# Kernel optimization log

Measured on AMD Instinct MI355X. Metric: run time of the kernel, lower is better.

## Reference

```python
import jax, jax.numpy as jnp
import numpy as np

B = 128      # trees per batch
D = 10       # tree depth (perfect binary tree)
L = 2 ** D   # leaves per tree
V = 50000    # vocab
E = 300      # embed size
C = 5        # num classes


def setup_inputs() -> dict:
    key = jax.random.key(0)
    k0, k1, k2, k3 = jax.random.split(key, 4)
    return {
        "word_ids": jax.random.randint(k0, (B, L), 0, V),
        "embedding": jax.random.normal(k1, (V, E), jnp.float32) * 0.02,
        "W_w": jax.random.normal(k2, (E, 2 * E), jnp.float32) * (1.0 / np.sqrt(2 * E)),
        "W_b": jnp.zeros((E,), jnp.float32),
        "P_w": jax.random.normal(k3, (C, E), jnp.float32) * (1.0 / np.sqrt(E)),
        "P_b": jnp.zeros((C,), jnp.float32),
    }


def reference(word_ids, embedding, W_w, W_b, P_w, P_b):
    # Leaf nodes: relu(Embedding(word))  -> [B, L, E]
    h = jax.nn.relu(embedding[word_ids])
    # projection of every node (torch Linear: x @ W.T + b)
    logits = [jnp.einsum("bne,ce->bnc", h, P_w) + P_b]
    # Combine same-depth sibling pairs level by level (D fixed levels).
    for _ in range(D):
        pair = jnp.concatenate([h[:, 0::2], h[:, 1::2]], axis=-1)  # [B, n/2, 2E]
        h = jax.nn.relu(jnp.einsum("bnf,ef->bne", pair, W_w) + W_b)  # [B, n/2, E]
        logits.append(jnp.einsum("bne,ce->bnc", h, P_w) + P_b)
    # All node logits, leaves first then each internal level up to the root.
    return jnp.concatenate(logits, axis=1)  # [B, 2L-1, C]
```

## Files before the change

kernel.cpp:

```cpp
#include <hip/hip_runtime.h>
#include <hip/hip_bf16.h>

#define B_ 128
#define D_ 10
#define L_ 1024
#define E_ 300
#define C_ 5
#define NODES 2047
#define HSTR 304
#define KP 608
#define NP 320
#define PK 320
#define LSTR 328

typedef __attribute__((ext_vector_type(8))) short short8;
typedef __attribute__((ext_vector_type(4))) float f32x4;
typedef __hip_bfloat16 bf16;

__device__ __forceinline__ short f2bs(float v) {
  bf16 b = (bf16)v;
  return *reinterpret_cast<short*>(&b);
}

__device__ __forceinline__ short8 pack_relu(f32x4 v0, f32x4 v1) {
  short8 s;
#pragma unroll
  for (int j = 0; j < 4; j++) s[j] = f2bs(fmaxf(v0[j], 0.f));
#pragma unroll
  for (int j = 0; j < 4; j++) s[4 + j] = f2bs(fmaxf(v1[j], 0.f));
  return s;
}

__global__ __launch_bounds__(256) void prep_k(
    const float* __restrict__ emb, const float* __restrict__ Ww,
    const float* __restrict__ Pw, bf16* __restrict__ T, bf16* __restrict__ Wp,
    bf16* __restrict__ Pp, bf16* __restrict__ Pq, int V) {
  int idx = blockIdx.x * 256 + threadIdx.x;
  int tchunks = V * 38;
  if (idx < tchunks) {
    int v = idx / 38, c = idx % 38;
    const float* src = emb + (size_t)v * E_ + c * 8;
    f32x4 v0 = *(const f32x4*)src;
    f32x4 v1;
    if (c == 37) v1 = (f32x4){0.f, 0.f, 0.f, 0.f};
    else v1 = *(const f32x4*)(src + 4);
    *(short8*)(T + (size_t)v * HSTR + c * 8) = pack_relu(v0, v1);
  }
  if (idx < NP * KP) {
    int r = idx / KP, c = idx % KP;
    float v = 0.f;
    if (r < E_) {
      if (c < E_) v = Ww[r * 600 + c];
      else if (c >= HSTR && c < HSTR + E_) v = Ww[r * 600 + (c - 4)];
    }
    Wp[idx] = (bf16)v;
  }
  if (idx < 16 * PK) {
    int r = idx / PK, c = idx % PK;
    float v = (r < C_ && c < E_) ? Pw[r * E_ + c] : 0.f;
    Pp[idx] = (bf16)v;
  }
  if (idx < 2 * 16 * KP) {
    int p = idx / (16 * KP);
    int rem = idx % (16 * KP);
    int r = rem / KP, c = rem % KP;
    int e = c - p * HSTR;
    float v = (r < C_ && e >= 0 && e < E_) ? Pw[r * E_ + e] : 0.f;
    Pq[idx] = (bf16)v;
  }
}

#define PROJ_A(rowptr, ks, k0)                                        \
  ((ks) == 9 && half >= 2 ? (short8){0, 0, 0, 0, 0, 0, 0, 0}          \
                          : *(const short8*)((rowptr) + (k0)))

__global__ __launch_bounds__(256, 4) void fused_l1_k(
    const int* __restrict__ wid, const bf16* __restrict__ T,
    const bf16* __restrict__ Wp, const float* __restrict__ Wb,
    const bf16* __restrict__ Pq, const bf16* __restrict__ Pp,
    const float* __restrict__ Pb, bf16* __restrict__ h1,
    float* __restrict__ out) {
  __shared__ bf16 hs[33][HSTR];
  int tid = threadIdx.x;
  int w = tid >> 6, l = tid & 63, q = l & 15, half = l >> 4;
  int m0 = blockIdx.x * 32;

  int mr0 = m0 + q, mr1 = m0 + 16 + q;
  int o0a = wid[2 * mr0] * HSTR, o0b = wid[2 * mr0 + 1] * HSTR;
  int o1a = wid[2 * mr1] * HSTR, o1b = wid[2 * mr1 + 1] * HSTR;

  int p = w & 1, rtl = w >> 1;

  f32x4 acc[2][5];
#pragma unroll
  for (int rt = 0; rt < 2; rt++)
#pragma unroll
    for (int nt = 0; nt < 5; nt++) acc[rt][nt] = (f32x4){0.f, 0.f, 0.f, 0.f};
  f32x4 pacc = (f32x4){0.f, 0.f, 0.f, 0.f};

#define LDA(ks, d0, d1)                                          \
  {                                                              \
    int k0_ = (ks) * 32 + half * 8;                              \
    int sel_ = k0_ >= HSTR;                                      \
    int e0_ = sel_ ? k0_ - HSTR : k0_;                           \
    d0 = *(const short8*)(T + (sel_ ? o0b : o0a) + e0_);         \
    d1 = *(const short8*)(T + (sel_ ? o1b : o1a) + e0_);         \
  }

  short8 aA0, aA1, aB0, aB1, aC0, aC1;
  LDA(0, aA0, aA1);
  LDA(1, aB0, aB1);

  for (int ks = 0; ks < 19; ks++) {
    int kn = ks + 2 <= 18 ? ks + 2 : 18;
    LDA(kn, aC0, aC1);
    int k0 = ks * 32 + half * 8;
    short8 al = rtl ? aA1 : aA0;
    short8 pqf = *(const short8*)(Pq + ((size_t)p * 16 + q) * KP + k0);
    pacc = __builtin_amdgcn_mfma_f32_16x16x32_bf16(al, pqf, pacc, 0, 0, 0);
#pragma unroll
    for (int nt = 0; nt < 5; nt++) {
      short8 b =
          *(const short8*)(Wp + (size_t)(w * 80 + nt * 16 + q) * KP + k0);
      acc[0][nt] =
          __builtin_amdgcn_mfma_f32_16x16x32_bf16(aA0, b, acc[0][nt], 0, 0, 0);
      acc[1][nt] =
          __builtin_amdgcn_mfma_f32_16x16x32_bf16(aA1, b, acc[1][nt], 0, 0, 0);
    }
    aA0 = aB0; aA1 = aB1;
    aB0 = aC0; aB1 = aC1;
  }
#undef LDA

#pragma unroll
  for (int nt = 0; nt < 5; nt++) {
    int n = w * 80 + nt * 16 + q;
    float wb = (n < E_) ? Wb[n] : 0.f;
    if (n < HSTR) {
#pragma unroll
      for (int rt = 0; rt < 2; rt++)
#pragma unroll
        for (int j = 0; j < 4; j++) {
          int rl = rt * 16 + half * 4 + j;
          hs[rl][n] = (bf16)fmaxf(acc[rt][nt][j] + wb, 0.f);
        }
    }
  }
  if (q < C_) {
    float pb = Pb[q];
#pragma unroll
    for (int j = 0; j < 4; j++) {
      int leaf = 2 * (m0 + rtl * 16 + half * 4 + j) + p;
      out[((size_t)(leaf >> 10) * NODES + (leaf & 1023)) * C_ + q] =
          pacc[j] + pb;
    }
  }
  __syncthreads();

  for (int i = tid; i < 32 * 38; i += 256) {
    int r = i / 38, c = i % 38;
    *(short8*)(h1 + (size_t)(m0 + r) * HSTR + c * 8) =
        *(const short8*)&hs[r][c * 8];
  }
  if (w < 2) {
    f32x4 pc = (f32x4){0.f, 0.f, 0.f, 0.f};
#pragma unroll
    for (int ks = 0; ks < 10; ks++) {
      int k0 = ks * 32 + half * 8;
      short8 a = PROJ_A(&hs[w * 16 + q][0], ks, k0);
      short8 b = *(const short8*)(Pp + (size_t)q * PK + k0);
      pc = __builtin_amdgcn_mfma_f32_16x16x32_bf16(a, b, pc, 0, 0, 0);
    }
    if (q < C_) {
      float pb = Pb[q];
#pragma unroll
      for (int j = 0; j < 4; j++) {
        int m = m0 + w * 16 + half * 4 + j;
        out[((size_t)(m >> 9) * NODES + 1024 + (m & 511)) * C_ + q] =
            pc[j] + pb;
      }
    }
  }
}

template <int RT>
__global__ __launch_bounds__(256, 4) void combine_k(
    const bf16* __restrict__ h_in, const bf16* __restrict__ Wp,
    const float* __restrict__ Wb, const bf16* __restrict__ Pp,
    const float* __restrict__ Pb, bf16* __restrict__ h_out,
    float* __restrict__ out, int node_off, int nshift) {
  __shared__ bf16 hs[RT * 16 + 1][HSTR];
  int tid = threadIdx.x;
  int w = tid >> 6, l = tid & 63, q = l & 15, half = l >> 4;
  size_t m0 = (size_t)blockIdx.x * (RT * 16);

  f32x4 acc[RT][5];
#pragma unroll
  for (int rt = 0; rt < RT; rt++)
#pragma unroll
    for (int nt = 0; nt < 5; nt++) acc[rt][nt] = (f32x4){0.f, 0.f, 0.f, 0.f};

  for (int ks = 0; ks < 19; ks++) {
    int k0 = ks * 32 + half * 8;
    short8 a[RT];
#pragma unroll
    for (int rt = 0; rt < RT; rt++)
      a[rt] = *(const short8*)(h_in + (m0 + rt * 16 + q) * KP + k0);
#pragma unroll
    for (int nt = 0; nt < 5; nt++) {
      short8 b =
          *(const short8*)(Wp + (size_t)(w * 80 + nt * 16 + q) * KP + k0);
#pragma unroll
      for (int rt = 0; rt < RT; rt++)
        acc[rt][nt] = __builtin_amdgcn_mfma_f32_16x16x32_bf16(a[rt], b,
                                                              acc[rt][nt], 0,
                                                              0, 0);
    }
  }

#pragma unroll
  for (int nt = 0; nt < 5; nt++) {
    int n = w * 80 + nt * 16 + q;
    float wb = (n < E_) ? Wb[n] : 0.f;
    if (n < HSTR) {
#pragma unroll
      for (int rt = 0; rt < RT; rt++)
#pragma unroll
        for (int j = 0; j < 4; j++) {
          int rl = rt * 16 + half * 4 + j;
          hs[rl][n] = (bf16)fmaxf(acc[rt][nt][j] + wb, 0.f);
        }
    }
  }
  __syncthreads();

  for (int i = tid; i < RT * 16 * 38; i += 256) {
    int r = i / 38, c = i % 38;
    *(short8*)(h_out + (m0 + r) * HSTR + c * 8) = *(const short8*)&hs[r][c * 8];
  }

  if (w < RT) {
    f32x4 pacc = (f32x4){0.f, 0.f, 0.f, 0.f};
#pragma unroll
    for (int ks = 0; ks < 10; ks++) {
      int k0 = ks * 32 + half * 8;
      short8 a = PROJ_A(&hs[16 * w + q][0], ks, k0);
      short8 b = *(const short8*)(Pp + (size_t)q * PK + k0);
      pacc = __builtin_amdgcn_mfma_f32_16x16x32_bf16(a, b, pacc, 0, 0, 0);
    }
    if (q < C_) {
      float pb = Pb[q];
#pragma unroll
      for (int j = 0; j < 4; j++) {
        size_t m = m0 + w * 16 + half * 4 + j;
        size_t b_ = m >> nshift;
        size_t n = m & (((size_t)1 << nshift) - 1);
        out[((size_t)b_ * NODES + node_off + n) * C_ + q] = pacc[j] + pb;
      }
    }
  }
}

__global__ __launch_bounds__(256) void tail_k(
    const bf16* __restrict__ h5, const bf16* __restrict__ Wp,
    const float* __restrict__ Wb, const bf16* __restrict__ Pp,
    const float* __restrict__ Pb, float* __restrict__ out) {
  __shared__ bf16 bufs[2][32][LSTR];
  int tid = threadIdx.x, b = blockIdx.x;
  int w = tid >> 6, l = tid & 63, q = l & 15, half = l >> 4;

  for (int i = tid; i < 32 * 38; i += 256) {
    int r = i / 38, c = i % 38;
    *(short8*)&bufs[0][r][c * 8] =
        *(const short8*)(h5 + ((size_t)b * 32 + r) * HSTR + c * 8);
  }
  __syncthreads();

  int p = 0, off = 2016, Mo = 16;
  for (int lev = 0; lev < 5; lev++) {
    f32x4 acc[5];
#pragma unroll
    for (int t = 0; t < 5; t++) acc[t] = (f32x4){0.f, 0.f, 0.f, 0.f};
    for (int ks = 0; ks < 19; ks++) {
      int k0 = ks * 32 + half * 8;
      int sel = k0 >= HSTR;
      int e0 = k0 - (sel ? HSTR : 0);
      short8 a = *(const short8*)&bufs[p][2 * q + sel][e0];
#pragma unroll
      for (int t = 0; t < 5; t++) {
        int nt = w + 4 * t;
        short8 bfr = *(const short8*)(Wp + ((size_t)nt * 16 + q) * KP + k0);
        acc[t] =
            __builtin_amdgcn_mfma_f32_16x16x32_bf16(a, bfr, acc[t], 0, 0, 0);
      }
    }
    __syncthreads();
#pragma unroll
    for (int t = 0; t < 5; t++) {
      int nt = w + 4 * t;
      int n = nt * 16 + q;
      float wb = (n < E_) ? Wb[n] : 0.f;
#pragma unroll
      for (int j = 0; j < 4; j++) {
        int r = half * 4 + j;
        bufs[p ^ 1][r][n] = (bf16)fmaxf(acc[t][j] + wb, 0.f);
      }
    }
    __syncthreads();
    if (w == 0) {
      f32x4 pc = (f32x4){0.f, 0.f, 0.f, 0.f};
#pragma unroll
      for (int ks = 0; ks < 10; ks++) {
        int k0 = ks * 32 + half * 8;
        short8 a = *(const short8*)&bufs[p ^ 1][q][k0];
        short8 bfr = *(const short8*)(Pp + (size_t)q * PK + k0);
        pc = __builtin_amdgcn_mfma_f32_16x16x32_bf16(a, bfr, pc, 0, 0, 0);
      }
      if (q < C_) {
        float pb = Pb[q];
#pragma unroll
        for (int j = 0; j < 4; j++) {
          int r = half * 4 + j;
          if (r < Mo) out[((size_t)b * NODES + off + r) * C_ + q] = pc[j] + pb;
        }
      }
    }
    p ^= 1;
    off += Mo;
    Mo >>= 1;
  }
}

extern "C" void kernel_launch(void* const* d_in, const int* in_sizes, int n_in,
                              void* d_out, int out_size, void* d_ws,
                              size_t ws_size, hipStream_t stream) {
  const int* wid = (const int*)d_in[0];
  const float* emb = (const float*)d_in[1];
  const float* Ww = (const float*)d_in[2];
  const float* Wb = (const float*)d_in[3];
  const float* Pw = (const float*)d_in[4];
  const float* Pb = (const float*)d_in[5];
  float* out = (float*)d_out;
  int V = in_sizes[1] / E_;

  bf16* hA = (bf16*)d_ws;
  bf16* hB = hA + (size_t)B_ * 512 * HSTR;
  bf16* Wp = hB + (size_t)B_ * 256 * HSTR;
  bf16* Pp = Wp + (size_t)NP * KP;
  bf16* Pq = Pp + (size_t)16 * PK;
  bf16* T = Pq + (size_t)2 * 16 * KP;

  int tchunks = V * 38;
  prep_k<<<(tchunks + 255) / 256, 256, 0, stream>>>(emb, Ww, Pw, T, Wp, Pp, Pq,
                                                    V);
  fused_l1_k<<<(B_ * 512) / 32, 256, 0, stream>>>(wid, T, Wp, Wb, Pq, Pp, Pb,
                                                  hA, out);
  combine_k<2><<<1024, 256, 0, stream>>>(hA, Wp, Wb, Pp, Pb, hB, out, 1536, 8);
  combine_k<2><<<512, 256, 0, stream>>>(hB, Wp, Wb, Pp, Pb, hA, out, 1792, 7);
  combine_k<1><<<512, 256, 0, stream>>>(hA, Wp, Wb, Pp, Pb, hB, out, 1920, 6);
  combine_k<1><<<256, 256, 0, stream>>>(hB, Wp, Wb, Pp, Pb, hA, out, 1984, 5);
  tail_k<<<B_, 256, 0, stream>>>(hA, Wp, Wb, Pp, Pb, out);
}
```

Baseline: 238.9 us.

## Drop full-vocab embedding prep, gather leaves in-kernel, use MFMA-fragment layouts

The prep kernel no longer converts the whole 50000x300 embedding table to bf16. It now only packs W and P into MFMA-fragment-ordered buffers. The level-1 kernel gathers and ReLU-converts the needed embedding rows directly into LDS and processes 64 rows per block. Intermediate activations are written in fragment order so later levels read contiguous 16-byte chunks per lane, and combine tile sizes are doubled. This removes a large pass over the embedding table, at the cost of more LDS and register pressure and lower occupancy.

```diff
diff --git a/kernel.cpp b/kernel.cpp
--- a/kernel.cpp
+++ b/kernel.cpp
@@ -2,16 +2,9 @@
 #include <hip/hip_bf16.h>
 
 #define B_ 128
-#define D_ 10
-#define L_ 1024
 #define E_ 300
 #define C_ 5
 #define NODES 2047
-#define HSTR 304
-#define KP 608
-#define NP 320
-#define PK 320
-#define LSTR 328
 
 typedef __attribute__((ext_vector_type(8))) short short8;
 typedef __attribute__((ext_vector_type(4))) float f32x4;
@@ -31,118 +24,143 @@
   return s;
 }
 
-__global__ __launch_bounds__(256) void prep_k(
-    const float* __restrict__ emb, const float* __restrict__ Ww,
-    const float* __restrict__ Pw, bf16* __restrict__ T, bf16* __restrict__ Wp,
-    bf16* __restrict__ Pp, bf16* __restrict__ Pq, int V) {
+#define HSROW(base, r) ((base) + (r) * 312)
+
+#define PROJ_A(rowptr, ks, k0)                               \
+  ((ks) == 9 && half >= 2 ? (short8){0, 0, 0, 0, 0, 0, 0, 0} \
+                          : *(const short8*)((rowptr) + (k0)))
+
+__global__ __launch_bounds__(256) void prep_k(const float* __restrict__ Ww,
+                                              const float* __restrict__ Pw,
+                                              bf16* __restrict__ Wf,
+                                              bf16* __restrict__ Pqf,
+                                              bf16* __restrict__ Ppf) {
   int idx = blockIdx.x * 256 + threadIdx.x;
-  int tchunks = V * 38;
-  if (idx < tchunks) {
-    int v = idx / 38, c = idx % 38;
-    const float* src = emb + (size_t)v * E_ + c * 8;
+  if (idx < 20 * 19 * 64) {
+    int wnt = idx / 1216, rem = idx % 1216;
+    int ks = rem >> 6, l = rem & 63;
+    int n = wnt * 16 + (l & 15);
+    int k0 = ks * 32 + (l >> 4) * 8;
+    short8 v;
+#pragma unroll
+    for (int j = 0; j < 8; j++) {
+      int k = k0 + j;
+      float x = 0.f;
+      if (n < E_) {
+        if (k < E_) x = Ww[n * 600 + k];
+        else if (k >= 304 && k < 604) x = Ww[n * 600 + k - 4];
+      }
+      v[j] = f2bs(x);
+    }
+    *(short8*)(Wf + (size_t)idx * 8) = v;
+  }
+  if (idx < 2 * 19 * 64) {
+    int p = idx / 1216, rem = idx % 1216;
+    int ks = rem >> 6, l = rem & 63;
+    int q = l & 15;
+    int k0 = ks * 32 + (l >> 4) * 8;
+    short8 v;
+#pragma unroll
+    for (int j = 0; j < 8; j++) {
+      int e = k0 + j - 304 * p;
+      float x = (q < C_ && e >= 0 && e < E_) ? Pw[q * E_ + e] : 0.f;
+      v[j] = f2bs(x);
+    }
+    *(short8*)(Pqf + (size_t)idx * 8) = v;
+  }
+  if (idx < 10 * 64) {
+    int ks = idx >> 6, l = idx & 63;
+    int q = l & 15;
+    int k0 = ks * 32 + (l >> 4) * 8;
+    short8 v;
+#pragma unroll
+    for (int j = 0; j < 8; j++) {
+      int e = k0 + j;
+      float x = (q < C_ && e < E_) ? Pw[q * E_ + e] : 0.f;
+      v[j] = f2bs(x);
+    }
+    *(short8*)(Ppf + (size_t)idx * 8) = v;
+  }
+}
+
+__global__ __launch_bounds__(256, 2) void fused_l1_k(
+    const int* __restrict__ wid, const float* __restrict__ emb,
+    const bf16* __restrict__ Wf, const float* __restrict__ Wb,
+    const bf16* __restrict__ Pqf, const bf16* __restrict__ Ppf,
+    const float* __restrict__ Pb, bf16* __restrict__ h1f,
+    float* __restrict__ out) {
+  __shared__ short ldsA[64 * 616 + 64];
+  int tid = threadIdx.x;
+  int m0 = blockIdx.x * 64;
+
+#pragma unroll 2
+  for (int it = 0; it < 19; ++it) {
+    int i = it * 256 + tid;
+    int r = i / 76, c2 = i % 76;
+    int par = c2 >= 38 ? 1 : 0;
+    int c = c2 - 38 * par;
+    int word = wid[2 * (m0 + r) + par];
+    const float* src = emb + (size_t)word * E_ + c * 8;
     f32x4 v0 = *(const f32x4*)src;
-    f32x4 v1;
-    if (c == 37) v1 = (f32x4){0.f, 0.f, 0.f, 0.f};
-    else v1 = *(const f32x4*)(src + 4);
-    *(short8*)(T + (size_t)v * HSTR + c * 8) = pack_relu(v0, v1);
-  }
-  if (idx < NP * KP) {
-    int r = idx / KP, c = idx % KP;
-    float v = 0.f;
-    if (r < E_) {
-      if (c < E_) v = Ww[r * 600 + c];
-      else if (c >= HSTR && c < HSTR + E_) v = Ww[r * 600 + (c - 4)];
-    }
-    Wp[idx] = (bf16)v;
-  }
-  if (idx < 16 * PK) {
-    int r = idx / PK, c = idx % PK;
-    float v = (r < C_ && c < E_) ? Pw[r * E_ + c] : 0.f;
-    Pp[idx] = (bf16)v;
-  }
-  if (idx < 2 * 16 * KP) {
-    int p = idx / (16 * KP);
-    int rem = idx % (16 * KP);
-    int r = rem / KP, c = rem % KP;
-    int e = c - p * HSTR;
-    float v = (r < C_ && e >= 0 && e < E_) ? Pw[r * E_ + e] : 0.f;
-    Pq[idx] = (bf16)v;
-  }
-}
-
-#define PROJ_A(rowptr, ks, k0)                                        \
-  ((ks) == 9 && half >= 2 ? (short8){0, 0, 0, 0, 0, 0, 0, 0}          \
-                          : *(const short8*)((rowptr) + (k0)))
-
-__global__ __launch_bounds__(256, 4) void fused_l1_k(
-    const int* __restrict__ wid, const bf16* __restrict__ T,
-    const bf16* __restrict__ Wp, const float* __restrict__ Wb,
-    const bf16* __restrict__ Pq, const bf16* __restrict__ Pp,
-    const float* __restrict__ Pb, bf16* __restrict__ h1,
-    float* __restrict__ out) {
-  __shared__ bf16 hs[33][HSTR];
-  int tid = threadIdx.x;
+    f32x4 v1 = (c == 37) ? (f32x4){0.f, 0.f, 0.f, 0.f}
+                         : *(const f32x4*)(src + 4);
+    *(short8*)&ldsA[r * 616 + par * 304 + c * 8] = pack_relu(v0, v1);
+  }
+  __syncthreads();
+
   int w = tid >> 6, l = tid & 63, q = l & 15, half = l >> 4;
-  int m0 = blockIdx.x * 32;
-
-  int mr0 = m0 + q, mr1 = m0 + 16 + q;
-  int o0a = wid[2 * mr0] * HSTR, o0b = wid[2 * mr0 + 1] * HSTR;
-  int o1a = wid[2 * mr1] * HSTR, o1b = wid[2 * mr1 + 1] * HSTR;
-
-  int p = w & 1, rtl = w >> 1;
-
-  f32x4 acc[2][5];
-#pragma unroll
-  for (int rt = 0; rt < 2; rt++)
+  int ab0 = (0 * 16 + q) * 616;
+  int ab1 = (1 * 16 + q) * 616;
+  int ab2 = (2 * 16 + q) * 616;
+  int ab3 = (3 * 16 + q) * 616;
+
+  f32x4 acc[4][5];
+#pragma unroll
+  for (int rt = 0; rt < 4; rt++)
 #pragma unroll
     for (int nt = 0; nt < 5; nt++) acc[rt][nt] = (f32x4){0.f, 0.f, 0.f, 0.f};
-  f32x4 pacc = (f32x4){0.f, 0.f, 0.f, 0.f};
-
-#define LDA(ks, d0, d1)                                          \
-  {                                                              \
-    int k0_ = (ks) * 32 + half * 8;                              \
-    int sel_ = k0_ >= HSTR;                                      \
-    int e0_ = sel_ ? k0_ - HSTR : k0_;                           \
-    d0 = *(const short8*)(T + (sel_ ? o0b : o0a) + e0_);         \
-    d1 = *(const short8*)(T + (sel_ ? o1b : o1a) + e0_);         \
-  }
-
-  short8 aA0, aA1, aB0, aB1, aC0, aC1;
-  LDA(0, aA0, aA1);
-  LDA(1, aB0, aB1);
-
+  f32x4 pacc0 = (f32x4){0.f, 0.f, 0.f, 0.f};
+  f32x4 pacc1 = (f32x4){0.f, 0.f, 0.f, 0.f};
+
+#pragma unroll 2
   for (int ks = 0; ks < 19; ks++) {
-    int kn = ks + 2 <= 18 ? ks + 2 : 18;
-    LDA(kn, aC0, aC1);
     int k0 = ks * 32 + half * 8;
-    short8 al = rtl ? aA1 : aA0;
-    short8 pqf = *(const short8*)(Pq + ((size_t)p * 16 + q) * KP + k0);
-    pacc = __builtin_amdgcn_mfma_f32_16x16x32_bf16(al, pqf, pacc, 0, 0, 0);
+    short8 a0 = *(const short8*)&ldsA[ab0 + k0];
+    short8 a1 = *(const short8*)&ldsA[ab1 + k0];
+    short8 a2 = *(const short8*)&ldsA[ab2 + k0];
+    short8 a3 = *(const short8*)&ldsA[ab3 + k0];
+    short8 al = w == 0 ? a0 : (w == 1 ? a1 : (w == 2 ? a2 : a3));
+    short8 pq0 = *(const short8*)(Pqf + ((size_t)(0 * 19 + ks) * 64 + l) * 8);
+    short8 pq1 = *(const short8*)(Pqf + ((size_t)(1 * 19 + ks) * 64 + l) * 8);
+    pacc0 = __builtin_amdgcn_mfma_f32_16x16x32_bf16(al, pq0, pacc0, 0, 0, 0);
+    pacc1 = __builtin_amdgcn_mfma_f32_16x16x32_bf16(al, pq1, pacc1, 0, 0, 0);
 #pragma unroll
     for (int nt = 0; nt < 5; nt++) {
-      short8 b =
-          *(const short8*)(Wp + (size_t)(w * 80 + nt * 16 + q) * KP + k0);
+      short8 b = *(const short8*)(Wf +
+          ((size_t)((5 * w + nt) * 19 + ks) * 64 + l) * 8);
       acc[0][nt] =
-          __builtin_amdgcn_mfma_f32_16x16x32_bf16(aA0, b, acc[0][nt], 0, 0, 0);
+          __builtin_amdgcn_mfma_f32_16x16x32_bf16(a0, b, acc[0][nt], 0, 0, 0);
       acc[1][nt] =
-          __builtin_amdgcn_mfma_f32_16x16x32_bf16(aA1, b, acc[1][nt], 0, 0, 0);
-    }
-    aA0 = aB0; aA1 = aB1;
-    aB0 = aC0; aB1 = aC1;
-  }
-#undef LDA
+          __builtin_amdgcn_mfma_f32_16x16x32_bf16(a1, b, acc[1][nt], 0, 0, 0);
+      acc[2][nt] =
+          __builtin_amdgcn_mfma_f32_16x16x32_bf16(a2, b, acc[2][nt], 0, 0, 0);
+      acc[3][nt] =
+          __builtin_amdgcn_mfma_f32_16x16x32_bf16(a3, b, acc[3][nt], 0, 0, 0);
+    }
+  }
+  __syncthreads();
 
 #pragma unroll
   for (int nt = 0; nt < 5; nt++) {
     int n = w * 80 + nt * 16 + q;
     float wb = (n < E_) ? Wb[n] : 0.f;
-    if (n < HSTR) {
-#pragma unroll
-      for (int rt = 0; rt < 2; rt++)
+    if (n < 304) {
+#pragma unroll
+      for (int rt = 0; rt < 4; rt++)
 #pragma unroll
         for (int j = 0; j < 4; j++) {
           int rl = rt * 16 + half * 4 + j;
-          hs[rl][n] = (bf16)fmaxf(acc[rt][nt][j] + wb, 0.f);
+          HSROW(ldsA, rl)[n] = f2bs(fmaxf(acc[rt][nt][j] + wb, 0.f));
         }
     }
   }
@@ -150,49 +168,56 @@
     float pb = Pb[q];
 #pragma unroll
     for (int j = 0; j < 4; j++) {
-      int leaf = 2 * (m0 + rtl * 16 + half * 4 + j) + p;
-      out[((size_t)(leaf >> 10) * NODES + (leaf & 1023)) * C_ + q] =
-          pacc[j] + pb;
+      int row = m0 + w * 16 + half * 4 + j;
+      int leaf0 = 2 * row, leaf1 = 2 * row + 1;
+      out[((size_t)(leaf0 >> 10) * NODES + (leaf0 & 1023)) * C_ + q] =
+          pacc0[j] + pb;
+      out[((size_t)(leaf1 >> 10) * NODES + (leaf1 & 1023)) * C_ + q] =
+          pacc1[j] + pb;
     }
   }
   __syncthreads();
 
-  for (int i = tid; i < 32 * 38; i += 256) {
-    int r = i / 38, c = i % 38;
-    *(short8*)(h1 + (size_t)(m0 + r) * HSTR + c * 8) =
-        *(const short8*)&hs[r][c * 8];
-  }
-  if (w < 2) {
-    f32x4 pc = (f32x4){0.f, 0.f, 0.f, 0.f};
-#pragma unroll
-    for (int ks = 0; ks < 10; ks++) {
-      int k0 = ks * 32 + half * 8;
-      short8 a = PROJ_A(&hs[w * 16 + q][0], ks, k0);
-      short8 b = *(const short8*)(Pp + (size_t)q * PK + k0);
-      pc = __builtin_amdgcn_mfma_f32_16x16x32_bf16(a, b, pc, 0, 0, 0);
-    }
-    if (q < C_) {
-      float pb = Pb[q];
-#pragma unroll
-      for (int j = 0; j < 4; j++) {
-        int m = m0 + w * 16 + half * 4 + j;
-        out[((size_t)(m >> 9) * NODES + 1024 + (m & 511)) * C_ + q] =
-            pc[j] + pb;
-      }
+  for (int i = tid; i < 2 * 19 * 64; i += 256) {
+    int gl = i / 1216, rem = i % 1216;
+    int ks = rem >> 6, ll = rem & 63;
+    int qq = ll & 15, hh = ll >> 4;
+    int k0 = ks * 32 + hh * 8;
+    int sel = k0 >= 304 ? 1 : 0;
+    int e = k0 - 304 * sel;
+    int lr = 2 * (gl * 16 + qq) + sel;
+    short8 v = *(const short8*)&HSROW(ldsA, lr)[e];
+    *(short8*)(h1f + (((size_t)((m0 >> 5) + gl) * 19 + ks) * 64 + ll) * 8) = v;
+  }
+  f32x4 pc = (f32x4){0.f, 0.f, 0.f, 0.f};
+#pragma unroll
+  for (int ks = 0; ks < 10; ks++) {
+    int k0 = ks * 32 + half * 8;
+    short8 a = PROJ_A(HSROW(ldsA, 16 * w + q), ks, k0);
+    short8 b = *(const short8*)(Ppf + ((size_t)ks * 64 + l) * 8);
+    pc = __builtin_amdgcn_mfma_f32_16x16x32_bf16(a, b, pc, 0, 0, 0);
+  }
+  if (q < C_) {
+    float pb = Pb[q];
+#pragma unroll
+    for (int j = 0; j < 4; j++) {
+      int m = m0 + w * 16 + half * 4 + j;
+      out[((size_t)(m >> 9) * NODES + 1024 + (m & 511)) * C_ + q] = pc[j] + pb;
     }
   }
 }
 
 template <int RT>
-__global__ __launch_bounds__(256, 4) void combine_k(
-    const bf16* __restrict__ h_in, const bf16* __restrict__ Wp,
-    const float* __restrict__ Wb, const bf16* __restrict__ Pp,
-    const float* __restrict__ Pb, bf16* __restrict__ h_out,
+__global__ __launch_bounds__(256, RT == 4 ? 3 : 4) void combine_k(
+    const bf16* __restrict__ hin_f, const bf16* __restrict__ Wf,
+    const float* __restrict__ Wb, const bf16* __restrict__ Ppf,
+    const float* __restrict__ Pb, bf16* __restrict__ hout_f,
     float* __restrict__ out, int node_off, int nshift) {
-  __shared__ bf16 hs[RT * 16 + 1][HSTR];
+  __shared__ short hsO[RT * 16 * 312 + 64];
   int tid = threadIdx.x;
   int w = tid >> 6, l = tid & 63, q = l & 15, half = l >> 4;
-  size_t m0 = (size_t)blockIdx.x * (RT * 16);
+  int m0 = blockIdx.x * (RT * 16);
+  int g0 = m0 >> 4;
 
   f32x4 acc[RT][5];
 #pragma unroll
@@ -200,21 +225,21 @@
 #pragma unroll
     for (int nt = 0; nt < 5; nt++) acc[rt][nt] = (f32x4){0.f, 0.f, 0.f, 0.f};
 
+#pragma unroll 2
   for (int ks = 0; ks < 19; ks++) {
-    int k0 = ks * 32 + half * 8;
     short8 a[RT];
 #pragma unroll
     for (int rt = 0; rt < RT; rt++)
-      a[rt] = *(const short8*)(h_in + (m0 + rt * 16 + q) * KP + k0);
+      a[rt] = *(const short8*)(hin_f +
+          (((size_t)(g0 + rt) * 19 + ks) * 64 + l) * 8);
 #pragma unroll
     for (int nt = 0; nt < 5; nt++) {
-      short8 b =
-          *(const short8*)(Wp + (size_t)(w * 80 + nt * 16 + q) * KP + k0);
+      short8 b = *(const short8*)(Wf +
+          ((size_t)((5 * w + nt) * 19 + ks) * 64 + l) * 8);
 #pragma unroll
       for (int rt = 0; rt < RT; rt++)
-        acc[rt][nt] = __builtin_amdgcn_mfma_f32_16x16x32_bf16(a[rt], b,
-                                                              acc[rt][nt], 0,
-                                                              0, 0);
+        acc[rt][nt] = __builtin_amdgcn_mfma_f32_16x16x32_bf16(
+            a[rt], b, acc[rt][nt], 0, 0, 0);
     }
   }
 
@@ -222,30 +247,37 @@
   for (int nt = 0; nt < 5; nt++) {
     int n = w * 80 + nt * 16 + q;
     float wb = (n < E_) ? Wb[n] : 0.f;
-    if (n < HSTR) {
+    if (n < 304) {
 #pragma unroll
       for (int rt = 0; rt < RT; rt++)
 #pragma unroll
         for (int j = 0; j < 4; j++) {
           int rl = rt * 16 + half * 4 + j;
-          hs[rl][n] = (bf16)fmaxf(acc[rt][nt][j] + wb, 0.f);
+          HSROW(hsO, rl)[n] = f2bs(fmaxf(acc[rt][nt][j] + wb, 0.f));
         }
     }
   }
   __syncthreads();
 
-  for (int i = tid; i < RT * 16 * 38; i += 256) {
-    int r = i / 38, c = i % 38;
-    *(short8*)(h_out + (m0 + r) * HSTR + c * 8) = *(const short8*)&hs[r][c * 8];
-  }
-
+  for (int i = tid; i < (RT / 2) * 1216; i += 256) {
+    int gl = i / 1216, rem = i % 1216;
+    int ks = rem >> 6, ll = rem & 63;
+    int qq = ll & 15, hh = ll >> 4;
+    int k0 = ks * 32 + hh * 8;
+    int sel = k0 >= 304 ? 1 : 0;
+    int e = k0 - 304 * sel;
+    int lr = 2 * (gl * 16 + qq) + sel;
+    short8 v = *(const short8*)&HSROW(hsO, lr)[e];
+    *(short8*)(hout_f +
+               (((size_t)((m0 >> 5) + gl) * 19 + ks) * 64 + ll) * 8) = v;
+  }
   if (w < RT) {
     f32x4 pacc = (f32x4){0.f, 0.f, 0.f, 0.f};
 #pragma unroll
     for (int ks = 0; ks < 10; ks++) {
       int k0 = ks * 32 + half * 8;
-      short8 a = PROJ_A(&hs[16 * w + q][0], ks, k0);
-      short8 b = *(const short8*)(Pp + (size_t)q * PK + k0);
+      short8 a = PROJ_A(HSROW(hsO, 16 * w + q), ks, k0);
+      short8 b = *(const short8*)(Ppf + ((size_t)ks * 64 + l) * 8);
       pacc = __builtin_amdgcn_mfma_f32_16x16x32_bf16(a, b, pacc, 0, 0, 0);
     }
     if (q < C_) {
@@ -261,20 +293,13 @@
   }
 }
 
-__global__ __launch_bounds__(256) void tail_k(
-    const bf16* __restrict__ h5, const bf16* __restrict__ Wp,
-    const float* __restrict__ Wb, const bf16* __restrict__ Pp,
+__global__ __launch_bounds__(256, 4) void tail_k(
+    const bf16* __restrict__ h5f, const bf16* __restrict__ Wf,
+    const float* __restrict__ Wb, const bf16* __restrict__ Ppf,
     const float* __restrict__ Pb, float* __restrict__ out) {
-  __shared__ bf16 bufs[2][32][LSTR];
+  __shared__ short bufs[2][16 * 312 + 64];
   int tid = threadIdx.x, b = blockIdx.x;
   int w = tid >> 6, l = tid & 63, q = l & 15, half = l >> 4;
-
-  for (int i = tid; i < 32 * 38; i += 256) {
-    int r = i / 38, c = i % 38;
-    *(short8*)&bufs[0][r][c * 8] =
-        *(const short8*)(h5 + ((size_t)b * 32 + r) * HSTR + c * 8);
-  }
-  __syncthreads();
 
   int p = 0, off = 2016, Mo = 16;
   for (int lev = 0; lev < 5; lev++) {
@@ -282,28 +307,36 @@
 #pragma unroll
     for (int t = 0; t < 5; t++) acc[t] = (f32x4){0.f, 0.f, 0.f, 0.f};
     for (int ks = 0; ks < 19; ks++) {
-      int k0 = ks * 32 + half * 8;
-      int sel = k0 >= HSTR;
-      int e0 = k0 - (sel ? HSTR : 0);
-      short8 a = *(const short8*)&bufs[p][2 * q + sel][e0];
+      short8 a;
+      if (lev == 0) {
+        a = *(const short8*)(h5f + (((size_t)b * 19 + ks) * 64 + l) * 8);
+      } else {
+        int k0 = ks * 32 + half * 8;
+        int sel = k0 >= 304 ? 1 : 0;
+        int e = k0 - 304 * sel;
+        int rr = 2 * q + sel;
+        rr = rr > 15 ? 15 : rr;
+        a = *(const short8*)&HSROW(bufs[p], rr)[e];
+      }
 #pragma unroll
       for (int t = 0; t < 5; t++) {
-        int nt = w + 4 * t;
-        short8 bfr = *(const short8*)(Wp + ((size_t)nt * 16 + q) * KP + k0);
+        short8 bf = *(const short8*)(Wf +
+            ((size_t)((w + 4 * t) * 19 + ks) * 64 + l) * 8);
         acc[t] =
-            __builtin_amdgcn_mfma_f32_16x16x32_bf16(a, bfr, acc[t], 0, 0, 0);
+            __builtin_amdgcn_mfma_f32_16x16x32_bf16(a, bf, acc[t], 0, 0, 0);
       }
     }
     __syncthreads();
 #pragma unroll
     for (int t = 0; t < 5; t++) {
-      int nt = w + 4 * t;
-      int n = nt * 16 + q;
+      int n = (w + 4 * t) * 16 + q;
       float wb = (n < E_) ? Wb[n] : 0.f;
-#pragma unroll
-      for (int j = 0; j < 4; j++) {
-        int r = half * 4 + j;
-        bufs[p ^ 1][r][n] = (bf16)fmaxf(acc[t][j] + wb, 0.f);
+      if (n < 304) {
+#pragma unroll
+        for (int j = 0; j < 4; j++) {
+          int r = half * 4 + j;
+          HSROW(bufs[p ^ 1], r)[n] = f2bs(fmaxf(acc[t][j] + wb, 0.f));
+        }
       }
     }
     __syncthreads();
@@ -312,9 +345,9 @@
 #pragma unroll
       for (int ks = 0; ks < 10; ks++) {
         int k0 = ks * 32 + half * 8;
-        short8 a = *(const short8*)&bufs[p ^ 1][q][k0];
-        short8 bfr = *(const short8*)(Pp + (size_t)q * PK + k0);
-        pc = __builtin_amdgcn_mfma_f32_16x16x32_bf16(a, bfr, pc, 0, 0, 0);
+        short8 a = PROJ_A(HSROW(bufs[p ^ 1], q), ks, k0);
+        short8 bf = *(const short8*)(Ppf + ((size_t)ks * 64 + l) * 8);
+        pc = __builtin_amdgcn_mfma_f32_16x16x32_bf16(a, bf, pc, 0, 0, 0);
       }
       if (q < C_) {
         float pb = Pb[q];
@@ -341,23 +374,18 @@
   const float* Pw = (const float*)d_in[4];
   const float* Pb = (const float*)d_in[5];
   float* out = (float*)d_out;
-  int V = in_sizes[1] / E_;
 
   bf16* hA = (bf16*)d_ws;
-  bf16* hB = hA + (size_t)B_ * 512 * HSTR;
-  bf16* Wp = hB + (size_t)B_ * 256 * HSTR;
-  bf16* Pp = Wp + (size_t)NP * KP;
-  bf16* Pq = Pp + (size_t)16 * PK;
-  bf16* T = Pq + (size_t)2 * 16 * KP;
-
-  int tchunks = V * 38;
-  prep_k<<<(tchunks + 255) / 256, 256, 0, stream>>>(emb, Ww, Pw, T, Wp, Pp, Pq,
-                                                    V);
-  fused_l1_k<<<(B_ * 512) / 32, 256, 0, stream>>>(wid, T, Wp, Wb, Pq, Pp, Pb,
-                                                  hA, out);
-  combine_k<2><<<1024, 256, 0, stream>>>(hA, Wp, Wb, Pp, Pb, hB, out, 1536, 8);
-  combine_k<2><<<512, 256, 0, stream>>>(hB, Wp, Wb, Pp, Pb, hA, out, 1792, 7);
-  combine_k<1><<<512, 256, 0, stream>>>(hA, Wp, Wb, Pp, Pb, hB, out, 1920, 6);
-  combine_k<1><<<256, 256, 0, stream>>>(hB, Wp, Wb, Pp, Pb, hA, out, 1984, 5);
-  tail_k<<<B_, 256, 0, stream>>>(hA, Wp, Wb, Pp, Pb, out);
-}
+  bf16* hB = hA + (size_t)B_ * 512 * 304;
+  bf16* Wf = hB + (size_t)B_ * 256 * 304;
+  bf16* Pqf = Wf + (size_t)20 * 19 * 512;
+  bf16* Ppf = Pqf + (size_t)2 * 19 * 512;
+
+  prep_k<<<95, 256, 0, stream>>>(Ww, Pw, Wf, Pqf, Ppf);
+  fused_l1_k<<<1024, 256, 0, stream>>>(wid, emb, Wf, Wb, Pqf, Ppf, Pb, hA, out);
+  combine_k<4><<<512, 256, 0, stream>>>(hA, Wf, Wb, Ppf, Pb, hB, out, 1536, 8);
+  combine_k<4><<<256, 256, 0, stream>>>(hB, Wf, Wb, Ppf, Pb, hA, out, 1792, 7);
+  combine_k<2><<<256, 256, 0, stream>>>(hA, Wf, Wb, Ppf, Pb, hB, out, 1920, 6);
+  combine_k<2><<<128, 256, 0, stream>>>(hB, Wf, Wb, Ppf, Pb, hA, out, 1984, 5);
+  tail_k<<<B_, 256, 0, stream>>>(hA, Wf, Wb, Ppf, Pb, out);
+}
```

After: 327.8 us. 1.37x slower.
